# Kernel optimization log

Hardware: AMD Instinct MI355X
Metric: run time of the kernel (lower is better)

The kernel has to match this reference:

```python
import jax, jax.numpy as jnp
import numpy as np

N, E = 20000, 256000
NODE_DIM, EDGE_DIM = 128, 8
HID, HEADS, LAYERS = 64, 4, 3   # TransformerConv: out_channels per head = HID, concat=False
CLASSES, GRAPHS = 3, 64
HC = HEADS * HID


def setup_inputs() -> dict:
    key = jax.random.key(0)
    ks = iter(jax.random.split(key, 40))
    g = lambda shape, s=0.05: jax.random.normal(next(ks), shape, dtype=jnp.float32) * s
    z = lambda shape: jnp.zeros(shape, jnp.float32)
    return dict(
        x=jax.random.normal(next(ks), (N, NODE_DIM), dtype=jnp.float32),
        edge_attr=jax.random.normal(next(ks), (E, EDGE_DIM), dtype=jnp.float32),
        node_W=g((NODE_DIM, HID)), node_b=z((HID,)),
        e1_W=g((EDGE_DIM, HID)), e1_b=z((HID,)),
        e2_W=g((HID, HID)), e2_b=z((HID,)),
        Wq=g((LAYERS, HID, HC)), bq=z((LAYERS, HC)),
        Wk=g((LAYERS, HID, HC)), bk=z((LAYERS, HC)),
        Wv=g((LAYERS, HID, HC)), bv=z((LAYERS, HC)),
        We=g((LAYERS, HID, HC)),                      # lin_edge has bias=False in PyG
        Wskip=g((LAYERS, HID, HID)), bskip=z((LAYERS, HID)),
        ln_g=jnp.ones((LAYERS, HID), jnp.float32), ln_b=z((LAYERS, HID)),
        cls_W=g((HID, CLASSES)), cls_b=z((CLASSES,)),
        edge_index=jax.random.randint(next(ks), (2, E), 0, N),
        batch=jnp.sort(jax.random.randint(next(ks), (N,), 0, GRAPHS)),
    )


def _layer_norm(x, g, b, eps=1e-5):
    m = x.mean(-1, keepdims=True)
    v = x.var(-1, keepdims=True)
    return (x - m) * jax.lax.rsqrt(v + eps) * g + b


def reference(x, edge_attr, node_W, node_b, e1_W, e1_b, e2_W, e2_b,
              Wq, bq, Wk, bk, Wv, bv, We, Wskip, bskip, ln_g, ln_b,
              cls_W, cls_b, edge_index, batch):
    src, dst = edge_index[0], edge_index[1]          # messages flow src -> dst
    h = x @ node_W + node_b                          # [N, HID]
    e = jax.nn.relu(edge_attr @ e1_W + e1_b) @ e2_W + e2_b  # [E, HID]
    scale = 1.0 / jnp.sqrt(jnp.float32(HID))
    for l in range(LAYERS):                          # fixed small layer count
        res = h
        q = (h @ Wq[l] + bq[l]).reshape(N, HEADS, HID)
        k = (h @ Wk[l] + bk[l]).reshape(N, HEADS, HID)
        v = (h @ Wv[l] + bv[l]).reshape(N, HEADS, HID)
        ee = (e @ We[l]).reshape(E, HEADS, HID)      # per-layer edge projection
        kj = k[src] + ee                             # [E, H, C] irregular gather
        alpha = (q[dst] * kj).sum(-1) * scale        # [E, H]
        amax = jax.ops.segment_max(alpha, dst, num_segments=N)
        ea = jnp.exp(alpha - amax[dst])
        denom = jax.ops.segment_sum(ea, dst, num_segments=N)
        alpha = ea / denom[dst]                      # segment softmax over in-edges
        # dropout on alpha: identity in eval mode
        msg = (v[src] + ee) * alpha[..., None]       # [E, H, C]
        agg = jax.ops.segment_sum(msg, dst, num_segments=N)  # [N, H, C]
        conv = agg.mean(axis=1) + (res @ Wskip[l] + bskip[l])  # concat=False, root_weight
        h = jax.nn.relu(_layer_norm(conv + res, ln_g[l], ln_b[l]))
        # model-level dropout: identity in eval mode
    gsum = jax.ops.segment_sum(h, batch, num_segments=GRAPHS)
    gcnt = jax.ops.segment_sum(jnp.ones((N, 1), h.dtype), batch, num_segments=GRAPHS)
    pooled = gsum / jnp.maximum(gcnt, 1.0)           # global mean pool
    return jax.nn.log_softmax(pooled @ cls_W + cls_b, axis=-1)  # [GRAPHS, CLASSES]
```

## Files before the change

kernel.cpp:

```cpp
#include <hip/hip_runtime.h>
#include <hip/hip_bf16.h>
#include <math.h>

#define NN 20000
#define NE 256000
#define NODE_DIM_ 128
#define EDGE_DIM_ 8
#define HID 64
#define HEADS 4
#define NLAYERS 3
#define NCLASSES 3
#define NGRAPHS 64
#define HC 256
#define EB 64
#define EPB 16

typedef __hip_bfloat16 bf16;
using v8s = __attribute__((ext_vector_type(8))) short;
using u16x8 = __attribute__((ext_vector_type(8))) unsigned short;
using f32x4 = __attribute__((ext_vector_type(4))) float;

__device__ __forceinline__ float B2F(bf16 x) { return __bfloat162float(x); }
__device__ __forceinline__ bf16 F2B(float x) { return __float2bfloat16(x); }
__device__ __forceinline__ short F2BS(float x) {
    union { bf16 b; short s; } u; u.b = __float2bfloat16(x); return u.s;
}
__device__ __forceinline__ float U2F(unsigned short u) { return __uint_as_float(((unsigned)u) << 16); }
__device__ __forceinline__ int clampi(int x, int lo, int hi) { return min(max(x, lo), hi); }

__global__ void gt_write_const(float* out, int n, float val) {
    int i = blockIdx.x * blockDim.x + threadIdx.x;
    if (i < n) out[i] = val;
}

__global__ void gt_zero_i32(int* p, int n) {
    int i = blockIdx.x * blockDim.x + threadIdx.x;
    if (i < n) p[i] = 0;
}

__global__ void gt_prep_wqe(const float* __restrict__ Wq, const float* __restrict__ bq,
                            const float* __restrict__ bk, const float* __restrict__ bv,
                            const float* __restrict__ We,
                            float* __restrict__ Wqe, float* __restrict__ bias4) {
    int b = blockIdx.x;
    int l = b / 65, kk = b % 65;
    int t = threadIdx.x;
    int hh = t >> 6, d = t & 63;
    const float* Weh = We + (size_t)l * HID * HC + (size_t)d * HC + hh * 64;
    if (kk < 64) {
        const float* Wqr = Wq + (size_t)l * HID * HC + (size_t)kk * HC + hh * 64;
        float s = 0.f;
        for (int c = 0; c < 64; ++c) s += Wqr[c] * Weh[c];
        Wqe[(size_t)l * HID * HC + (size_t)kk * HC + t] = s;
    } else {
        const float* bqr = bq + (size_t)l * HC + hh * 64;
        float s = 0.f;
        for (int c = 0; c < 64; ++c) s += bqr[c] * Weh[c];
        bias4[(size_t)l * 1024 + 768 + t] = s;
        bias4[(size_t)l * 1024 + t]       = bq[(size_t)l * HC + t];
        bias4[(size_t)l * 1024 + 256 + t] = bk[(size_t)l * HC + t];
        bias4[(size_t)l * 1024 + 512 + t] = bv[(size_t)l * HC + t];
    }
}

__global__ void gt_pack_qkv(const float* __restrict__ Wq, const float* __restrict__ Wk,
                            const float* __restrict__ Wv, const float* __restrict__ Wqe,
                            bf16* __restrict__ Bp) {
    int idx = blockIdx.x * 256 + threadIdx.x;
    if (idx >= NLAYERS * 8192) return;
    int lane = idx & 63;
    int ks = (idx >> 6) & 1;
    int nf = (idx >> 7) & 63;
    int l = idx >> 13;
    int col = nf * 16 + (lane & 15);
    int k0 = ks * 32 + (lane >> 4) * 8;
    const float* src;
    int c;
    if (col < 256)      { src = Wq  + (size_t)l * HID * HC; c = col; }
    else if (col < 512) { src = Wk  + (size_t)l * HID * HC; c = col - 256; }
    else if (col < 768) { src = Wv  + (size_t)l * HID * HC; c = col - 512; }
    else                { src = Wqe + (size_t)l * HID * HC; c = col - 768; }
    bf16* dst = Bp + (size_t)idx * 8;
#pragma unroll
    for (int j = 0; j < 8; ++j) dst[j] = F2B(src[(size_t)(k0 + j) * HC + c]);
}

__global__ void gt_pack_w2(const float* __restrict__ W2, bf16* __restrict__ B2p) {
    int idx = blockIdx.x * 256 + threadIdx.x;
    if (idx >= 512) return;
    int lane = idx & 63;
    int ks = (idx >> 6) & 1;
    int nf = idx >> 7;
    int col = nf * 16 + (lane & 15);
    int k0 = ks * 32 + (lane >> 4) * 8;
    bf16* dst = B2p + (size_t)idx * 8;
#pragma unroll
    for (int j = 0; j < 8; ++j) dst[j] = F2B(W2[(size_t)(k0 + j) * HID + col]);
}

__global__ void gt_prep_wcomb(const float* __restrict__ We, const float* __restrict__ Wskip,
                              float* __restrict__ Wc) {
    int idx = blockIdx.x * blockDim.x + threadIdx.x;
    if (idx >= NLAYERS * 320 * 64) return;
    int l = idx / (320 * 64);
    int r = idx % (320 * 64);
    int kk = r / 64;
    int c = r % 64;
    float val;
    if (kk < 256) {
        int hh = kk >> 6, j = kk & 63;
        val = We[(size_t)l * HID * HC + (size_t)j * HC + hh * 64 + c];
    } else {
        int j = kk - 256;
        val = Wskip[(size_t)l * HID * HID + (size_t)j * HID + c];
    }
    Wc[(size_t)l * 320 * 64 + (size_t)((kk >> 2) * 64 + c) * 4 + (kk & 3)] = val;
}

__global__ void gt_node_proj(const float* __restrict__ x, const float* __restrict__ W,
                             const float* __restrict__ b, float* __restrict__ h) {
    int t = threadIdx.x;
    int n = blockIdx.x * 4 + (t >> 6);
    int c = t & 63;
    __shared__ float xr[4][NODE_DIM_];
    for (int i = t; i < 4 * NODE_DIM_; i += 256) {
        int nn = blockIdx.x * 4 + i / NODE_DIM_;
        xr[i / NODE_DIM_][i % NODE_DIM_] = (nn < NN) ? x[(size_t)nn * NODE_DIM_ + i % NODE_DIM_] : 0.f;
    }
    __syncthreads();
    if (n >= NN) return;
    float acc = 0.f;
#pragma unroll 8
    for (int j = 0; j < NODE_DIM_; ++j) acc += xr[t >> 6][j] * W[j * HID + c];
    h[(size_t)n * HID + c] = acc + b[c];
}

__global__ void gt_edge_mlp(const float* __restrict__ ea, const float* __restrict__ W1,
                            const float* __restrict__ b1, const bf16* __restrict__ B2p,
                            const float* __restrict__ b2, bf16* __restrict__ ef) {
    int t = threadIdx.x;
    int c = t & 63, slot = t >> 6;
    int e0 = blockIdx.x * EB;
    __shared__ float aS[EB][EDGE_DIM_];
    __shared__ bf16 t1s[EB * 64];
    for (int i = t; i < EB * EDGE_DIM_; i += 256) {
        ((float*)aS)[i] = ea[(size_t)e0 * EDGE_DIM_ + i];
    }
    float w1r[EDGE_DIM_];
#pragma unroll
    for (int j = 0; j < EDGE_DIM_; ++j) w1r[j] = W1[j * HID + c];
    float b1c = b1[c];
    __syncthreads();
    int cu = c >> 3, ci = c & 7;
#pragma unroll
    for (int es16 = 0; es16 < 16; ++es16) {
        int es = slot * 16 + es16;
        float acc = b1c;
#pragma unroll
        for (int j = 0; j < EDGE_DIM_; ++j) acc += aS[es][j] * w1r[j];
        int cs = ((cu ^ (es & 7)) << 3) | ci;
        t1s[es * 64 + cs] = F2B(fmaxf(acc, 0.f));
    }
    __syncthreads();
    int lane = t & 63, wave = slot;
    v8s bfr0 = *(const v8s*)(B2p + ((size_t)(wave * 2 + 0) * 64 + lane) * 8);
    v8s bfr1 = *(const v8s*)(B2p + ((size_t)(wave * 2 + 1) * 64 + lane) * 8);
    int rowA = lane & 15, kg = lane >> 4;
    f32x4 acc[4];
#pragma unroll
    for (int mf = 0; mf < 4; ++mf) acc[mf] = (f32x4){0.f, 0.f, 0.f, 0.f};
#pragma unroll
    for (int mf = 0; mf < 4; ++mf) {
        int r = mf * 16 + rowA;
        int u0 = 0 * 4 + kg, u1 = 1 * 4 + kg;
        v8s a0 = *(const v8s*)&t1s[r * 64 + ((u0 ^ (r & 7)) << 3)];
        v8s a1 = *(const v8s*)&t1s[r * 64 + ((u1 ^ (r & 7)) << 3)];
        acc[mf] = __builtin_amdgcn_mfma_f32_16x16x32_bf16(a0, bfr0, acc[mf], 0, 0, 0);
        acc[mf] = __builtin_amdgcn_mfma_f32_16x16x32_bf16(a1, bfr1, acc[mf], 0, 0, 0);
    }
    int col = wave * 16 + (lane & 15);
    float bb = b2[col];
    int rbase = (lane >> 4) * 4;
#pragma unroll
    for (int mf = 0; mf < 4; ++mf) {
#pragma unroll
        for (int reg = 0; reg < 4; ++reg) {
            int e = e0 + mf * 16 + rbase + reg;
            ef[(size_t)e * HID + col] = F2B(acc[mf][reg] + bb);
        }
    }
}

__global__ void gt_count_dst(const int* __restrict__ ei, int* cnt) {
    int e = blockIdx.x * blockDim.x + threadIdx.x;
    if (e < NE) {
        int d = clampi(ei[NE + e], 0, NN - 1);
        atomicAdd(&cnt[d], 1);
    }
}

__global__ void gt_scan_csr(const int* __restrict__ cnt, int* __restrict__ rp, int* __restrict__ cur) {
    __shared__ int part[256];
    int tid = threadIdx.x;
    const int CH = (NN + 255) / 256;
    int s0 = tid * CH, s1 = min(s0 + CH, NN);
    int s = 0;
    for (int i = s0; i < s1; ++i) s += cnt[i];
    part[tid] = s;
    __syncthreads();
    for (int off = 1; off < 256; off <<= 1) {
        int vv = (tid >= off) ? part[tid - off] : 0;
        __syncthreads();
        if (tid >= off) part[tid] += vv;
        __syncthreads();
    }
    int base = (tid == 0) ? 0 : part[tid - 1];
    for (int i = s0; i < s1; ++i) {
        rp[i] = base;
        cur[i] = base;
        base += cnt[i];
    }
    if (tid == 255) rp[NN] = part[255];
}

__global__ void gt_fill_csr(const int* __restrict__ ei, int* cur, int* csr) {
    int e = blockIdx.x * blockDim.x + threadIdx.x;
    if (e < NE) {
        int d = clampi(ei[NE + e], 0, NN - 1);
        int pos = atomicAdd(&cur[d], 1);
        if (pos >= 0 && pos < NE) csr[pos] = e;
    }
}

__global__ void __launch_bounds__(256)
gt_qkv_mfma(const float* __restrict__ h, const bf16* __restrict__ Bp,
            const float* __restrict__ bias4,
            float* __restrict__ q, bf16* __restrict__ kv, float* __restrict__ qe) {
    int t = threadIdx.x, lane = t & 63, wave = t >> 6;
    int n0 = blockIdx.x * 16;
    int rowA = lane & 15, kg = lane >> 4;

    v8s a[2];
    {
        const float* hr = h + (size_t)(n0 + rowA) * HID;
#pragma unroll
        for (int ks = 0; ks < 2; ++ks) {
            const float* p = hr + ks * 32 + kg * 8;
            float4 x0 = *(const float4*)p;
            float4 x1 = *(const float4*)(p + 4);
            v8s av;
            av[0] = F2BS(x0.x); av[1] = F2BS(x0.y); av[2] = F2BS(x0.z); av[3] = F2BS(x0.w);
            av[4] = F2BS(x1.x); av[5] = F2BS(x1.y); av[6] = F2BS(x1.z); av[7] = F2BS(x1.w);
            a[ks] = av;
        }
    }

    f32x4 acc[16];
#pragma unroll
    for (int nf = 0; nf < 16; ++nf) acc[nf] = (f32x4){0.f, 0.f, 0.f, 0.f};

#pragma unroll
    for (int nf = 0; nf < 16; ++nf) {
        int nfg = wave * 16 + nf;
        v8s b0 = *(const v8s*)(Bp + ((size_t)(nfg * 2 + 0) * 64 + lane) * 8);
        v8s b1 = *(const v8s*)(Bp + ((size_t)(nfg * 2 + 1) * 64 + lane) * 8);
        acc[nf] = __builtin_amdgcn_mfma_f32_16x16x32_bf16(a[0], b0, acc[nf], 0, 0, 0);
        acc[nf] = __builtin_amdgcn_mfma_f32_16x16x32_bf16(a[1], b1, acc[nf], 0, 0, 0);
    }

    int rbase = (lane >> 4) * 4;
#pragma unroll
    for (int nf = 0; nf < 16; ++nf) {
        int cc = nf * 16 + (lane & 15);
        float bias = bias4[wave * 256 + cc];
#pragma unroll
        for (int reg = 0; reg < 4; ++reg) {
            int n = n0 + rbase + reg;
            float val = acc[nf][reg] + bias;
            if (wave == 0)      q [(size_t)n * HC + cc] = val;
            else if (wave == 1) kv[(size_t)n * 512 + ((cc >> 2) << 3) + (cc & 3)] = F2B(val);
            else if (wave == 2) kv[(size_t)n * 512 + ((cc >> 2) << 3) + 4 + (cc & 3)] = F2B(val);
            else                qe[(size_t)n * HC + cc] = val;
        }
    }
}

__global__ void gt_attn_core(float* __restrict__ q, float* __restrict__ qe,
                             const bf16* __restrict__ kv, const bf16* __restrict__ ef,
                             const int* __restrict__ rp, const int* __restrict__ csr,
                             const int* __restrict__ ei) {
    int t = threadIdx.x;
    int lane = t & 63, wave = t >> 6;
    int n = blockIdx.x * 4 + wave;
    if (n >= NN) return;

    const float4* q4 = (const float4*)q;
    const float4* qe4 = (const float4*)qe;
    const u16x8* kv8 = (const u16x8*)kv;
    const ushort4* e4p = (const ushort4*)ef;
    int elane = lane & 15;

    float4 qv = q4[(size_t)n * 64 + lane];
    float4 qev = qe4[(size_t)n * 64 + lane];

    int s0 = clampi(rp[n], 0, NE), s1 = clampi(rp[n + 1], s0, NE);
    float m = -1e30f, lr = 0.f;
    float4 accv = make_float4(0.f, 0.f, 0.f, 0.f);
    float4 accs = make_float4(0.f, 0.f, 0.f, 0.f);

    auto process = [&](u16x8 k0, ushort4 f0, u16x8 k1, ushort4 f1, bool ok0, bool ok1) {
        float p0 = qv.x * U2F(k0[0]) + qv.y * U2F(k0[1]) + qv.z * U2F(k0[2]) + qv.w * U2F(k0[3])
                 + qev.x * U2F(f0.x) + qev.y * U2F(f0.y) + qev.z * U2F(f0.z) + qev.w * U2F(f0.w);
        float p1 = qv.x * U2F(k1[0]) + qv.y * U2F(k1[1]) + qv.z * U2F(k1[2]) + qv.w * U2F(k1[3])
                 + qev.x * U2F(f1.x) + qev.y * U2F(f1.y) + qev.z * U2F(f1.z) + qev.w * U2F(f1.w);
        p0 += __shfl_xor(p0, 8, 16);  p1 += __shfl_xor(p1, 8, 16);
        p0 += __shfl_xor(p0, 4, 16);  p1 += __shfl_xor(p1, 4, 16);
        p0 += __shfl_xor(p0, 2, 16);  p1 += __shfl_xor(p1, 2, 16);
        p0 += __shfl_xor(p0, 1, 16);  p1 += __shfl_xor(p1, 1, 16);
        p0 = ok0 ? p0 * 0.125f : -1e30f;
        p1 = ok1 ? p1 * 0.125f : -1e30f;
        float pm = fmaxf(p0, p1);
        if (__any(pm - m > 8.f)) {
            float nm = fmaxf(m, pm);
            float sc = __expf(m - nm);
            m = nm;
            lr *= sc;
            accv.x *= sc; accv.y *= sc; accv.z *= sc; accv.w *= sc;
            accs.x *= sc; accs.y *= sc; accs.z *= sc; accs.w *= sc;
        }
        float w0 = __expf(p0 - m);
        float w1 = __expf(p1 - m);
        lr += w0 + w1;
        accv.x += w0 * U2F(k0[4]) + w1 * U2F(k1[4]);
        accv.y += w0 * U2F(k0[5]) + w1 * U2F(k1[5]);
        accv.z += w0 * U2F(k0[6]) + w1 * U2F(k1[6]);
        accv.w += w0 * U2F(k0[7]) + w1 * U2F(k1[7]);
        accs.x += w0 * U2F(f0.x) + w1 * U2F(f1.x);
        accs.y += w0 * U2F(f0.y) + w1 * U2F(f1.y);
        accs.z += w0 * U2F(f0.z) + w1 * U2F(f1.z);
        accs.w += w0 * U2F(f0.w) + w1 * U2F(f1.w);
    };

    for (int base = s0; base < s1; base += 64) {
        int cnt = min(64, s1 - base);
        int eL = 0, srcL = 0;
        if (lane < cnt) {
            eL = clampi(csr[base + lane], 0, NE - 1);
            srcL = clampi(ei[eL], 0, NN - 1);
        }
        int jb = min(1, cnt - 1);
        int eA0 = __builtin_amdgcn_readlane(eL, 0), rA0 = __builtin_amdgcn_readlane(srcL, 0);
        int eA1 = __builtin_amdgcn_readlane(eL, jb), rA1 = __builtin_amdgcn_readlane(srcL, jb);
        u16x8 kvA0 = kv8[(size_t)rA0 * 64 + lane];
        u16x8 kvA1 = kv8[(size_t)rA1 * 64 + lane];
        ushort4 efA0 = e4p[(size_t)eA0 * 16 + elane];
        ushort4 efA1 = e4p[(size_t)eA1 * 16 + elane];
        u16x8 kvB0, kvB1;
        ushort4 efB0, efB1;
        for (int i = 0; i < cnt; i += 4) {
            {
                int j2 = min(i + 2, cnt - 1), j3 = min(i + 3, cnt - 1);
                int e2 = __builtin_amdgcn_readlane(eL, j2), r2 = __builtin_amdgcn_readlane(srcL, j2);
                int e3 = __builtin_amdgcn_readlane(eL, j3), r3 = __builtin_amdgcn_readlane(srcL, j3);
                kvB0 = kv8[(size_t)r2 * 64 + lane];
                kvB1 = kv8[(size_t)r3 * 64 + lane];
                efB0 = e4p[(size_t)e2 * 16 + elane];
                efB1 = e4p[(size_t)e3 * 16 + elane];
            }
            process(kvA0, efA0, kvA1, efA1, true, i + 1 < cnt);
            if (i + 4 < cnt) {
                int j4 = i + 4, j5 = min(i + 5, cnt - 1);
                int e4 = __builtin_amdgcn_readlane(eL, j4), r4 = __builtin_amdgcn_readlane(srcL, j4);
                int e5 = __builtin_amdgcn_readlane(eL, j5), r5 = __builtin_amdgcn_readlane(srcL, j5);
                kvA0 = kv8[(size_t)r4 * 64 + lane];
                kvA1 = kv8[(size_t)r5 * 64 + lane];
                efA0 = e4p[(size_t)e4 * 16 + elane];
                efA1 = e4p[(size_t)e5 * 16 + elane];
            }
            if (i + 2 < cnt) {
                process(kvB0, efB0, kvB1, efB1, true, i + 3 < cnt);
            }
        }
    }
    float inv = (s1 > s0) ? 0.25f / lr : 0.f;
    float4 rs = make_float4(accs.x * inv, accs.y * inv, accs.z * inv, accs.w * inv);
    ((float4*)q)[(size_t)n * 64 + lane] = rs;
    float4 rv = make_float4(accv.x * inv, accv.y * inv, accv.z * inv, accv.w * inv);
    rv.x += __shfl_xor(rv.x, 16, 64); rv.x += __shfl_xor(rv.x, 32, 64);
    rv.y += __shfl_xor(rv.y, 16, 64); rv.y += __shfl_xor(rv.y, 32, 64);
    rv.z += __shfl_xor(rv.z, 16, 64); rv.z += __shfl_xor(rv.z, 32, 64);
    rv.w += __shfl_xor(rv.w, 16, 64); rv.w += __shfl_xor(rv.w, 32, 64);
    if (lane < 16) ((float4*)qe)[(size_t)n * 64 + lane] = rv;
}

__global__ void gt_epilogue(const float* __restrict__ acc_s, const float* __restrict__ acc_vm,
                            const float* __restrict__ Wc, const float* __restrict__ bskip,
                            const float* __restrict__ lng, const float* __restrict__ lnb,
                            float* __restrict__ h) {
    int t = threadIdx.x;
    int c = t & 63, qw = t >> 6;
    int n0 = blockIdx.x * EPB;
    __shared__ float sK[EPB][320];
    __shared__ float sVM[EPB][64];
    const float4* as4 = (const float4*)acc_s;
    for (int i = t; i < EPB * 64; i += 256) {
        int nd = i >> 6, j4 = i & 63;
        *(float4*)&sK[nd][4 * j4] = as4[(size_t)(n0 + nd) * 64 + j4];
    }
    const float4* h4g = (const float4*)h;
    const float4* vm4 = (const float4*)acc_vm;
    for (int i = t; i < EPB * 16; i += 256) {
        int nd = i >> 4, j4 = i & 15;
        *(float4*)&sK[nd][256 + 4 * j4] = h4g[(size_t)(n0 + nd) * 16 + j4];
        *(float4*)&sVM[nd][4 * j4] = vm4[(size_t)(n0 + nd) * 64 + j4];
    }
    __syncthreads();
    int nb = qw * 4;
    const float4* r0 = (const float4*)&sK[nb][0];
    const float4* r1 = (const float4*)&sK[nb + 1][0];
    const float4* r2 = (const float4*)&sK[nb + 2][0];
    const float4* r3 = (const float4*)&sK[nb + 3][0];
    const float4* W4 = (const float4*)Wc;
    float a0 = 0.f, a1 = 0.f, a2 = 0.f, a3 = 0.f;
#pragma unroll 4
    for (int k4 = 0; k4 < 80; ++k4) {
        float4 w = W4[k4 * 64 + c];
        float4 x0 = r0[k4]; a0 += x0.x * w.x + x0.y * w.y + x0.z * w.z + x0.w * w.w;
        float4 x1 = r1[k4]; a1 += x1.x * w.x + x1.y * w.y + x1.z * w.z + x1.w * w.w;
        float4 x2 = r2[k4]; a2 += x2.x * w.x + x2.y * w.y + x2.z * w.z + x2.w * w.w;
        float4 x3 = r3[k4]; a3 += x3.x * w.x + x3.y * w.y + x3.z * w.z + x3.w * w.w;
    }
    float bsk = bskip[c], g = lng[c], bb = lnb[c];
    float y0 = a0 + sVM[nb][c] + sK[nb][256 + c] + bsk;
    float y1 = a1 + sVM[nb + 1][c] + sK[nb + 1][256 + c] + bsk;
    float y2 = a2 + sVM[nb + 2][c] + sK[nb + 2][256 + c] + bsk;
    float y3 = a3 + sVM[nb + 3][c] + sK[nb + 3][256 + c] + bsk;
    float m0 = y0, m1 = y1, m2 = y2, m3 = y3;
#pragma unroll
    for (int s = 32; s > 0; s >>= 1) {
        m0 += __shfl_xor(m0, s, 64);
        m1 += __shfl_xor(m1, s, 64);
        m2 += __shfl_xor(m2, s, 64);
        m3 += __shfl_xor(m3, s, 64);
    }
    m0 *= (1.f / HID); m1 *= (1.f / HID); m2 *= (1.f / HID); m3 *= (1.f / HID);
    float d0 = y0 - m0, d1 = y1 - m1, d2 = y2 - m2, d3 = y3 - m3;
    float v0 = d0 * d0, v1 = d1 * d1, v2 = d2 * d2, v3 = d3 * d3;
#pragma unroll
    for (int s = 32; s > 0; s >>= 1) {
        v0 += __shfl_xor(v0, s, 64);
        v1 += __shfl_xor(v1, s, 64);
        v2 += __shfl_xor(v2, s, 64);
        v3 += __shfl_xor(v3, s, 64);
    }
    v0 *= (1.f / HID); v1 *= (1.f / HID); v2 *= (1.f / HID); v3 *= (1.f / HID);
    h[(size_t)(n0 + nb) * HID + c]     = fmaxf(d0 * rsqrtf(v0 + 1e-5f) * g + bb, 0.f);
    h[(size_t)(n0 + nb + 1) * HID + c] = fmaxf(d1 * rsqrtf(v1 + 1e-5f) * g + bb, 0.f);
    h[(size_t)(n0 + nb + 2) * HID + c] = fmaxf(d2 * rsqrtf(v2 + 1e-5f) * g + bb, 0.f);
    h[(size_t)(n0 + nb + 3) * HID + c] = fmaxf(d3 * rsqrtf(v3 + 1e-5f) * g + bb, 0.f);
}

__global__ void gt_pool_sum(const float* __restrict__ h, const int* __restrict__ batch,
                            float* __restrict__ psum) {
    int t = threadIdx.x;
    int c = t & 63, slot = t >> 6;
    int n0 = blockIdx.x * 256;
    float acc = 0.f;
    int curg = -1;
    for (int i = slot; i < 256; i += 4) {
        int n = n0 + i;
        if (n >= NN) break;
        int g = clampi(batch[n], 0, NGRAPHS - 1);
        float val = h[(size_t)n * HID + c];
        if (g != curg) {
            if (curg >= 0) atomicAdd(&psum[curg * HID + c], acc);
            curg = g;
            acc = 0.f;
        }
        acc += val;
    }
    if (curg >= 0) atomicAdd(&psum[curg * HID + c], acc);
}

__global__ void gt_classify(const float* __restrict__ psum, const int* __restrict__ batch,
                            const float* __restrict__ W, const float* __restrict__ b,
                            float* __restrict__ out) {
    int g = blockIdx.x;
    int c = threadIdx.x;
    __shared__ float pooled[HID];
    __shared__ float lg[4];
    __shared__ int bounds[2];
    if (c < 2) {
        int target = g + c;
        int lo = 0, hi = NN;
        while (lo < hi) {
            int mid = (lo + hi) >> 1;
            if (batch[mid] < target) lo = mid + 1; else hi = mid;
        }
        bounds[c] = lo;
    }
    __syncthreads();
    float divf = fmaxf((float)(bounds[1] - bounds[0]), 1.f);
    pooled[c] = psum[g * HID + c] / divf;
    __syncthreads();
    if (c < NCLASSES) {
        float acc = 0.f;
        for (int j = 0; j < HID; ++j) acc += pooled[j] * W[j * NCLASSES + c];
        lg[c] = acc + b[c];
    }
    __syncthreads();
    if (c == 0) {
        float m = fmaxf(lg[0], fmaxf(lg[1], lg[2]));
        float ssum = 0.f;
        for (int cc = 0; cc < NCLASSES; ++cc) ssum += __expf(lg[cc] - m);
        float lse = logf(ssum);
        for (int cc = 0; cc < NCLASSES; ++cc) out[g * NCLASSES + cc] = lg[cc] - m - lse;
    }
}

extern "C" void kernel_launch(void* const* d_in, const int* in_sizes, int n_in,
                              void* d_out, int out_size, void* d_ws, size_t ws_size,
                              hipStream_t stream) {
    float* out = (float*)d_out;

    static const int EXPECT[23] = {2560000, 2048000, 8192, 64, 512, 64, 4096, 64,
                                   49152, 768, 49152, 768, 49152, 768, 49152,
                                   12288, 192, 192, 192, 192, 3, 512000, 20000};
    int bad = -1;
    if (n_in != 23) bad = 99;
    else {
        for (int i = 0; i < 23; ++i) {
            if (in_sizes[i] != EXPECT[i]) { bad = i; break; }
        }
    }
    if (bad >= 0) {
        float val = (bad == 99) ? 4000.f : (5000.f + 10.f * bad);
        gt_write_const<<<1, 256, 0, stream>>>(out, out_size, val);
        return;
    }

    const float* x        = (const float*)d_in[0];
    const float* edge_attr= (const float*)d_in[1];
    const float* node_W   = (const float*)d_in[2];
    const float* node_b   = (const float*)d_in[3];
    const float* e1_W     = (const float*)d_in[4];
    const float* e1_b     = (const float*)d_in[5];
    const float* e2_W     = (const float*)d_in[6];
    const float* e2_b     = (const float*)d_in[7];
    const float* Wq       = (const float*)d_in[8];
    const float* bq       = (const float*)d_in[9];
    const float* Wk       = (const float*)d_in[10];
    const float* bk       = (const float*)d_in[11];
    const float* Wv       = (const float*)d_in[12];
    const float* bv       = (const float*)d_in[13];
    const float* We       = (const float*)d_in[14];
    const float* Wskip    = (const float*)d_in[15];
    const float* bskip    = (const float*)d_in[16];
    const float* lng      = (const float*)d_in[17];
    const float* lnb      = (const float*)d_in[18];
    const float* cls_W    = (const float*)d_in[19];
    const float* cls_b    = (const float*)d_in[20];
    const int*   ei       = (const int*)d_in[21];
    const int*   batch    = (const int*)d_in[22];

    char* w = (char*)d_ws;
    auto alloc = [&](size_t bytes) -> char* {
        char* p = w;
        w += (bytes + 255) & ~(size_t)255;
        return p;
    };
    float* h     = (float*)alloc((size_t)NN * HID * 4);
    bf16*  ef    = (bf16*)alloc((size_t)NE * HID * 2);
    float* q     = (float*)alloc((size_t)NN * HC * 4);
    bf16*  kv    = (bf16*)alloc((size_t)NN * 512 * 2);
    float* qe    = (float*)alloc((size_t)NN * HC * 4);
    float* Wqe   = (float*)alloc((size_t)NLAYERS * HID * HC * 4);
    float* bias4 = (float*)alloc((size_t)NLAYERS * 1024 * 4);
    bf16*  Bp    = (bf16*)alloc((size_t)NLAYERS * 8192 * 8 * 2);
    bf16*  B2p   = (bf16*)alloc((size_t)512 * 8 * 2);
    float* Wc    = (float*)alloc((size_t)NLAYERS * 320 * 64 * 4);
    float* psum  = (float*)alloc((size_t)NGRAPHS * HID * 4);
    int*   cnt   = (int*)alloc((size_t)NN * 4);
    int*   rp    = (int*)alloc((size_t)(NN + 1) * 4);
    int*   cur   = (int*)alloc((size_t)NN * 4);
    int*   csr   = (int*)alloc((size_t)NE * 4);

    gt_node_proj<<<(NN + 3) / 4, 256, 0, stream>>>(x, node_W, node_b, h);
    gt_prep_wqe<<<NLAYERS * 65, 256, 0, stream>>>(Wq, bq, bk, bv, We, Wqe, bias4);
    gt_pack_qkv<<<(NLAYERS * 8192 + 255) / 256, 256, 0, stream>>>(Wq, Wk, Wv, Wqe, Bp);
    gt_pack_w2<<<2, 256, 0, stream>>>(e2_W, B2p);
    gt_edge_mlp<<<NE / EB, 256, 0, stream>>>(edge_attr, e1_W, e1_b, B2p, e2_b, ef);
    gt_prep_wcomb<<<(NLAYERS * 320 * 64 + 255) / 256, 256, 0, stream>>>(We, Wskip, Wc);
    gt_zero_i32<<<(NN + 255) / 256, 256, 0, stream>>>(cnt, NN);
    gt_count_dst<<<(NE + 255) / 256, 256, 0, stream>>>(ei, cnt);
    gt_scan_csr<<<1, 256, 0, stream>>>(cnt, rp, cur);
    gt_fill_csr<<<(NE + 255) / 256, 256, 0, stream>>>(ei, cur, csr);

    for (int l = 0; l < NLAYERS; ++l) {
        const bf16* Bp_l  = Bp + (size_t)l * 8192 * 8;
        const float* b4_l = bias4 + (size_t)l * 1024;
        const float* Wc_l = Wc + (size_t)l * 320 * 64;
        const float* bs_l = bskip + (size_t)l * HID;
        const float* lg_l = lng + (size_t)l * HID;
        const float* lb_l = lnb + (size_t)l * HID;

        gt_qkv_mfma<<<NN / 16, 256, 0, stream>>>(h, Bp_l, b4_l, q, kv, qe);
        gt_attn_core<<<(NN + 3) / 4, 256, 0, stream>>>(q, qe, kv, ef, rp, csr, ei);
        gt_epilogue<<<NN / EPB, 256, 0, stream>>>(q, qe, Wc_l, bs_l, lg_l, lb_l, h);
    }

    gt_zero_i32<<<(NGRAPHS * HID + 255) / 256, 256, 0, stream>>>((int*)psum, NGRAPHS * HID);
    gt_pool_sum<<<(NN + 255) / 256, 256, 0, stream>>>(h, batch, psum);
    gt_classify<<<NGRAPHS, HID, 0, stream>>>(psum, batch, cls_W, cls_b, out);
}
```

Measured before the change: 558.2 us.

## Fuse attention aggregation with skip-projection, layer norm and ReLU epilogue

Merges the attention core and the epilogue kernel into one kernel, so each wave finishes its node's aggregation in registers and LDS and then runs the combined skip/edge projection, layer norm and ReLU itself. This removes one launch per layer and the global round-trip of the aggregated buffers. The edge loop now prefetches eight edges at a time and keeps two independent accumulator sets to expose more memory-level parallelism. In exchange, register pressure rises, and the Wc weights are now read once per node rather than once per 16 nodes, though they are likely cache-resident.

```diff
diff --git a/kernel.cpp b/kernel.cpp
--- a/kernel.cpp
+++ b/kernel.cpp
@@ -13,7 +13,6 @@
 #define NGRAPHS 64
 #define HC 256
 #define EB 64
-#define EPB 16
 
 typedef __hip_bfloat16 bf16;
 using v8s = __attribute__((ext_vector_type(8))) short;
@@ -285,14 +284,18 @@
     }
 }
 
-__global__ void gt_attn_core(float* __restrict__ q, float* __restrict__ qe,
-                             const bf16* __restrict__ kv, const bf16* __restrict__ ef,
-                             const int* __restrict__ rp, const int* __restrict__ csr,
-                             const int* __restrict__ ei) {
+__global__ void gt_attn_fused(const float* __restrict__ q, const float* __restrict__ qe,
+                              const bf16* __restrict__ kv, const bf16* __restrict__ ef,
+                              const int* __restrict__ rp, const int* __restrict__ csr,
+                              const int* __restrict__ ei, const float* __restrict__ Wc,
+                              const float* __restrict__ bskip, const float* __restrict__ lng,
+                              const float* __restrict__ lnb, float* __restrict__ h) {
     int t = threadIdx.x;
     int lane = t & 63, wave = t >> 6;
     int n = blockIdx.x * 4 + wave;
-    if (n >= NN) return;
+
+    __shared__ float sS[4][320];
+    __shared__ float sVM[4][64];
 
     const float4* q4 = (const float4*)q;
     const float4* qe4 = (const float4*)qe;
@@ -302,17 +305,20 @@
 
     float4 qv = q4[(size_t)n * 64 + lane];
     float4 qev = qe4[(size_t)n * 64 + lane];
+    float resc = h[(size_t)n * HID + lane];
 
     int s0 = clampi(rp[n], 0, NE), s1 = clampi(rp[n + 1], s0, NE);
-    float m = -1e30f, lr = 0.f;
-    float4 accv = make_float4(0.f, 0.f, 0.f, 0.f);
-    float4 accs = make_float4(0.f, 0.f, 0.f, 0.f);
-
-    auto process = [&](u16x8 k0, ushort4 f0, u16x8 k1, ushort4 f1, bool ok0, bool ok1) {
-        float p0 = qv.x * U2F(k0[0]) + qv.y * U2F(k0[1]) + qv.z * U2F(k0[2]) + qv.w * U2F(k0[3])
-                 + qev.x * U2F(f0.x) + qev.y * U2F(f0.y) + qev.z * U2F(f0.z) + qev.w * U2F(f0.w);
-        float p1 = qv.x * U2F(k1[0]) + qv.y * U2F(k1[1]) + qv.z * U2F(k1[2]) + qv.w * U2F(k1[3])
-                 + qev.x * U2F(f1.x) + qev.y * U2F(f1.y) + qev.z * U2F(f1.z) + qev.w * U2F(f1.w);
+    float m = -1e30f;
+    float lrA = 0.f, lrB = 0.f;
+    float4 avA = make_float4(0.f, 0.f, 0.f, 0.f), asA = make_float4(0.f, 0.f, 0.f, 0.f);
+    float4 avB = make_float4(0.f, 0.f, 0.f, 0.f), asB = make_float4(0.f, 0.f, 0.f, 0.f);
+
+    auto proc2 = [&](const u16x8& K0, const ushort4& F0, const u16x8& K1, const ushort4& F1,
+                     bool ok0, bool ok1, float& lr_, float4& av_, float4& as_) {
+        float p0 = qv.x * U2F(K0[0]) + qv.y * U2F(K0[1]) + qv.z * U2F(K0[2]) + qv.w * U2F(K0[3])
+                 + qev.x * U2F(F0.x) + qev.y * U2F(F0.y) + qev.z * U2F(F0.z) + qev.w * U2F(F0.w);
+        float p1 = qv.x * U2F(K1[0]) + qv.y * U2F(K1[1]) + qv.z * U2F(K1[2]) + qv.w * U2F(K1[3])
+                 + qev.x * U2F(F1.x) + qev.y * U2F(F1.y) + qev.z * U2F(F1.z) + qev.w * U2F(F1.w);
         p0 += __shfl_xor(p0, 8, 16);  p1 += __shfl_xor(p1, 8, 16);
         p0 += __shfl_xor(p0, 4, 16);  p1 += __shfl_xor(p1, 4, 16);
         p0 += __shfl_xor(p0, 2, 16);  p1 += __shfl_xor(p1, 2, 16);
@@ -324,21 +330,23 @@
             float nm = fmaxf(m, pm);
             float sc = __expf(m - nm);
             m = nm;
-            lr *= sc;
-            accv.x *= sc; accv.y *= sc; accv.z *= sc; accv.w *= sc;
-            accs.x *= sc; accs.y *= sc; accs.z *= sc; accs.w *= sc;
+            lrA *= sc; lrB *= sc;
+            avA.x *= sc; avA.y *= sc; avA.z *= sc; avA.w *= sc;
+            asA.x *= sc; asA.y *= sc; asA.z *= sc; asA.w *= sc;
+            avB.x *= sc; avB.y *= sc; avB.z *= sc; avB.w *= sc;
+            asB.x *= sc; asB.y *= sc; asB.z *= sc; asB.w *= sc;
         }
         float w0 = __expf(p0 - m);
         float w1 = __expf(p1 - m);
-        lr += w0 + w1;
-        accv.x += w0 * U2F(k0[4]) + w1 * U2F(k1[4]);
-        accv.y += w0 * U2F(k0[5]) + w1 * U2F(k1[5]);
-        accv.z += w0 * U2F(k0[6]) + w1 * U2F(k1[6]);
-        accv.w += w0 * U2F(k0[7]) + w1 * U2F(k1[7]);
-        accs.x += w0 * U2F(f0.x) + w1 * U2F(f1.x);
-        accs.y += w0 * U2F(f0.y) + w1 * U2F(f1.y);
-        accs.z += w0 * U2F(f0.z) + w1 * U2F(f1.z);
-        accs.w += w0 * U2F(f0.w) + w1 * U2F(f1.w);
+        lr_ += w0 + w1;
+        av_.x += w0 * U2F(K0[4]) + w1 * U2F(K1[4]);
+        av_.y += w0 * U2F(K0[5]) + w1 * U2F(K1[5]);
+        av_.z += w0 * U2F(K0[6]) + w1 * U2F(K1[6]);
+        av_.w += w0 * U2F(K0[7]) + w1 * U2F(K1[7]);
+        as_.x += w0 * U2F(F0.x) + w1 * U2F(F1.x);
+        as_.y += w0 * U2F(F0.y) + w1 * U2F(F1.y);
+        as_.z += w0 * U2F(F0.z) + w1 * U2F(F1.z);
+        as_.w += w0 * U2F(F0.w) + w1 * U2F(F1.w);
     };
 
     for (int base = s0; base < s1; base += 64) {
@@ -348,116 +356,78 @@
             eL = clampi(csr[base + lane], 0, NE - 1);
             srcL = clampi(ei[eL], 0, NN - 1);
         }
-        int jb = min(1, cnt - 1);
-        int eA0 = __builtin_amdgcn_readlane(eL, 0), rA0 = __builtin_amdgcn_readlane(srcL, 0);
-        int eA1 = __builtin_amdgcn_readlane(eL, jb), rA1 = __builtin_amdgcn_readlane(srcL, jb);
-        u16x8 kvA0 = kv8[(size_t)rA0 * 64 + lane];
-        u16x8 kvA1 = kv8[(size_t)rA1 * 64 + lane];
-        ushort4 efA0 = e4p[(size_t)eA0 * 16 + elane];
-        ushort4 efA1 = e4p[(size_t)eA1 * 16 + elane];
-        u16x8 kvB0, kvB1;
-        ushort4 efB0, efB1;
-        for (int i = 0; i < cnt; i += 4) {
-            {
-                int j2 = min(i + 2, cnt - 1), j3 = min(i + 3, cnt - 1);
-                int e2 = __builtin_amdgcn_readlane(eL, j2), r2 = __builtin_amdgcn_readlane(srcL, j2);
-                int e3 = __builtin_amdgcn_readlane(eL, j3), r3 = __builtin_amdgcn_readlane(srcL, j3);
-                kvB0 = kv8[(size_t)r2 * 64 + lane];
-                kvB1 = kv8[(size_t)r3 * 64 + lane];
-                efB0 = e4p[(size_t)e2 * 16 + elane];
-                efB1 = e4p[(size_t)e3 * 16 + elane];
+        int i1 = min(1, cnt - 1), i2 = min(2, cnt - 1), i3 = min(3, cnt - 1);
+        int e0 = __builtin_amdgcn_readlane(eL, 0),  r0 = __builtin_amdgcn_readlane(srcL, 0);
+        int e1 = __builtin_amdgcn_readlane(eL, i1), r1 = __builtin_amdgcn_readlane(srcL, i1);
+        int e2 = __builtin_amdgcn_readlane(eL, i2), r2 = __builtin_amdgcn_readlane(srcL, i2);
+        int e3 = __builtin_amdgcn_readlane(eL, i3), r3 = __builtin_amdgcn_readlane(srcL, i3);
+        u16x8 K10 = kv8[(size_t)r0 * 64 + lane], K11 = kv8[(size_t)r1 * 64 + lane];
+        u16x8 K12 = kv8[(size_t)r2 * 64 + lane], K13 = kv8[(size_t)r3 * 64 + lane];
+        ushort4 F10 = e4p[(size_t)e0 * 16 + elane], F11 = e4p[(size_t)e1 * 16 + elane];
+        ushort4 F12 = e4p[(size_t)e2 * 16 + elane], F13 = e4p[(size_t)e3 * 16 + elane];
+        for (int i = 0; i < cnt; i += 8) {
+            int j4 = min(i + 4, cnt - 1), j5 = min(i + 5, cnt - 1);
+            int j6 = min(i + 6, cnt - 1), j7 = min(i + 7, cnt - 1);
+            int e4 = __builtin_amdgcn_readlane(eL, j4), r4 = __builtin_amdgcn_readlane(srcL, j4);
+            int e5 = __builtin_amdgcn_readlane(eL, j5), r5 = __builtin_amdgcn_readlane(srcL, j5);
+            int e6 = __builtin_amdgcn_readlane(eL, j6), r6 = __builtin_amdgcn_readlane(srcL, j6);
+            int e7 = __builtin_amdgcn_readlane(eL, j7), r7 = __builtin_amdgcn_readlane(srcL, j7);
+            u16x8 K20 = kv8[(size_t)r4 * 64 + lane], K21 = kv8[(size_t)r5 * 64 + lane];
+            u16x8 K22 = kv8[(size_t)r6 * 64 + lane], K23 = kv8[(size_t)r7 * 64 + lane];
+            ushort4 F20 = e4p[(size_t)e4 * 16 + elane], F21 = e4p[(size_t)e5 * 16 + elane];
+            ushort4 F22 = e4p[(size_t)e6 * 16 + elane], F23 = e4p[(size_t)e7 * 16 + elane];
+            proc2(K10, F10, K11, F11, true, i + 1 < cnt, lrA, avA, asA);
+            proc2(K12, F12, K13, F13, i + 2 < cnt, i + 3 < cnt, lrB, avB, asB);
+            if (i + 8 < cnt) {
+                int j9 = min(i + 9, cnt - 1), j10 = min(i + 10, cnt - 1), j11 = min(i + 11, cnt - 1);
+                int e8 = __builtin_amdgcn_readlane(eL, i + 8), r8 = __builtin_amdgcn_readlane(srcL, i + 8);
+                int e9 = __builtin_amdgcn_readlane(eL, j9),    r9 = __builtin_amdgcn_readlane(srcL, j9);
+                int eA = __builtin_amdgcn_readlane(eL, j10),   rA = __builtin_amdgcn_readlane(srcL, j10);
+                int eB = __builtin_amdgcn_readlane(eL, j11),   rB = __builtin_amdgcn_readlane(srcL, j11);
+                K10 = kv8[(size_t)r8 * 64 + lane]; K11 = kv8[(size_t)r9 * 64 + lane];
+                K12 = kv8[(size_t)rA * 64 + lane]; K13 = kv8[(size_t)rB * 64 + lane];
+                F10 = e4p[(size_t)e8 * 16 + elane]; F11 = e4p[(size_t)e9 * 16 + elane];
+                F12 = e4p[(size_t)eA * 16 + elane]; F13 = e4p[(size_t)eB * 16 + elane];
             }
-            process(kvA0, efA0, kvA1, efA1, true, i + 1 < cnt);
             if (i + 4 < cnt) {
-                int j4 = i + 4, j5 = min(i + 5, cnt - 1);
-                int e4 = __builtin_amdgcn_readlane(eL, j4), r4 = __builtin_amdgcn_readlane(srcL, j4);
-                int e5 = __builtin_amdgcn_readlane(eL, j5), r5 = __builtin_amdgcn_readlane(srcL, j5);
-                kvA0 = kv8[(size_t)r4 * 64 + lane];
-                kvA1 = kv8[(size_t)r5 * 64 + lane];
-                efA0 = e4p[(size_t)e4 * 16 + elane];
-                efA1 = e4p[(size_t)e5 * 16 + elane];
+                proc2(K20, F20, K21, F21, true, i + 5 < cnt, lrA, avA, asA);
+                proc2(K22, F22, K23, F23, i + 6 < cnt, i + 7 < cnt, lrB, avB, asB);
             }
-            if (i + 2 < cnt) {
-                process(kvB0, efB0, kvB1, efB1, true, i + 3 < cnt);
-            }
-        }
-    }
+        }
+    }
+    float lr = lrA + lrB;
     float inv = (s1 > s0) ? 0.25f / lr : 0.f;
-    float4 rs = make_float4(accs.x * inv, accs.y * inv, accs.z * inv, accs.w * inv);
-    ((float4*)q)[(size_t)n * 64 + lane] = rs;
-    float4 rv = make_float4(accv.x * inv, accv.y * inv, accv.z * inv, accv.w * inv);
+    float4 rs = make_float4((asA.x + asB.x) * inv, (asA.y + asB.y) * inv,
+                            (asA.z + asB.z) * inv, (asA.w + asB.w) * inv);
+    *(float4*)&sS[wave][4 * lane] = rs;
+    sS[wave][256 + lane] = resc;
+    float4 rv = make_float4((avA.x + avB.x) * inv, (avA.y + avB.y) * inv,
+                            (avA.z + avB.z) * inv, (avA.w + avB.w) * inv);
     rv.x += __shfl_xor(rv.x, 16, 64); rv.x += __shfl_xor(rv.x, 32, 64);
     rv.y += __shfl_xor(rv.y, 16, 64); rv.y += __shfl_xor(rv.y, 32, 64);
     rv.z += __shfl_xor(rv.z, 16, 64); rv.z += __shfl_xor(rv.z, 32, 64);
     rv.w += __shfl_xor(rv.w, 16, 64); rv.w += __shfl_xor(rv.w, 32, 64);
-    if (lane < 16) ((float4*)qe)[(size_t)n * 64 + lane] = rv;
-}
-
-__global__ void gt_epilogue(const float* __restrict__ acc_s, const float* __restrict__ acc_vm,
-                            const float* __restrict__ Wc, const float* __restrict__ bskip,
-                            const float* __restrict__ lng, const float* __restrict__ lnb,
-                            float* __restrict__ h) {
-    int t = threadIdx.x;
-    int c = t & 63, qw = t >> 6;
-    int n0 = blockIdx.x * EPB;
-    __shared__ float sK[EPB][320];
-    __shared__ float sVM[EPB][64];
-    const float4* as4 = (const float4*)acc_s;
-    for (int i = t; i < EPB * 64; i += 256) {
-        int nd = i >> 6, j4 = i & 63;
-        *(float4*)&sK[nd][4 * j4] = as4[(size_t)(n0 + nd) * 64 + j4];
-    }
-    const float4* h4g = (const float4*)h;
-    const float4* vm4 = (const float4*)acc_vm;
-    for (int i = t; i < EPB * 16; i += 256) {
-        int nd = i >> 4, j4 = i & 15;
-        *(float4*)&sK[nd][256 + 4 * j4] = h4g[(size_t)(n0 + nd) * 16 + j4];
-        *(float4*)&sVM[nd][4 * j4] = vm4[(size_t)(n0 + nd) * 64 + j4];
-    }
-    __syncthreads();
-    int nb = qw * 4;
-    const float4* r0 = (const float4*)&sK[nb][0];
-    const float4* r1 = (const float4*)&sK[nb + 1][0];
-    const float4* r2 = (const float4*)&sK[nb + 2][0];
-    const float4* r3 = (const float4*)&sK[nb + 3][0];
+    if (lane < 16) *(float4*)&sVM[wave][4 * lane] = rv;
+    __syncthreads();
     const float4* W4 = (const float4*)Wc;
-    float a0 = 0.f, a1 = 0.f, a2 = 0.f, a3 = 0.f;
+    float a = 0.f;
 #pragma unroll 4
     for (int k4 = 0; k4 < 80; ++k4) {
-        float4 w = W4[k4 * 64 + c];
-        float4 x0 = r0[k4]; a0 += x0.x * w.x + x0.y * w.y + x0.z * w.z + x0.w * w.w;
-        float4 x1 = r1[k4]; a1 += x1.x * w.x + x1.y * w.y + x1.z * w.z + x1.w * w.w;
-        float4 x2 = r2[k4]; a2 += x2.x * w.x + x2.y * w.y + x2.z * w.z + x2.w * w.w;
-        float4 x3 = r3[k4]; a3 += x3.x * w.x + x3.y * w.y + x3.z * w.z + x3.w * w.w;
-    }
-    float bsk = bskip[c], g = lng[c], bb = lnb[c];
-    float y0 = a0 + sVM[nb][c] + sK[nb][256 + c] + bsk;
-    float y1 = a1 + sVM[nb + 1][c] + sK[nb + 1][256 + c] + bsk;
-    float y2 = a2 + sVM[nb + 2][c] + sK[nb + 2][256 + c] + bsk;
-    float y3 = a3 + sVM[nb + 3][c] + sK[nb + 3][256 + c] + bsk;
-    float m0 = y0, m1 = y1, m2 = y2, m3 = y3;
-#pragma unroll
-    for (int s = 32; s > 0; s >>= 1) {
-        m0 += __shfl_xor(m0, s, 64);
-        m1 += __shfl_xor(m1, s, 64);
-        m2 += __shfl_xor(m2, s, 64);
-        m3 += __shfl_xor(m3, s, 64);
-    }
-    m0 *= (1.f / HID); m1 *= (1.f / HID); m2 *= (1.f / HID); m3 *= (1.f / HID);
-    float d0 = y0 - m0, d1 = y1 - m1, d2 = y2 - m2, d3 = y3 - m3;
-    float v0 = d0 * d0, v1 = d1 * d1, v2 = d2 * d2, v3 = d3 * d3;
-#pragma unroll
-    for (int s = 32; s > 0; s >>= 1) {
-        v0 += __shfl_xor(v0, s, 64);
-        v1 += __shfl_xor(v1, s, 64);
-        v2 += __shfl_xor(v2, s, 64);
-        v3 += __shfl_xor(v3, s, 64);
-    }
-    v0 *= (1.f / HID); v1 *= (1.f / HID); v2 *= (1.f / HID); v3 *= (1.f / HID);
-    h[(size_t)(n0 + nb) * HID + c]     = fmaxf(d0 * rsqrtf(v0 + 1e-5f) * g + bb, 0.f);
-    h[(size_t)(n0 + nb + 1) * HID + c] = fmaxf(d1 * rsqrtf(v1 + 1e-5f) * g + bb, 0.f);
-    h[(size_t)(n0 + nb + 2) * HID + c] = fmaxf(d2 * rsqrtf(v2 + 1e-5f) * g + bb, 0.f);
-    h[(size_t)(n0 + nb + 3) * HID + c] = fmaxf(d3 * rsqrtf(v3 + 1e-5f) * g + bb, 0.f);
+        float4 xk = *(const float4*)&sS[wave][4 * k4];
+        float4 w = W4[(size_t)k4 * 64 + lane];
+        a += xk.x * w.x + xk.y * w.y + xk.z * w.z + xk.w * w.w;
+    }
+    float y = a + sVM[wave][lane] + resc + bskip[lane];
+    float mm = y;
+#pragma unroll
+    for (int s = 32; s > 0; s >>= 1) mm += __shfl_xor(mm, s, 64);
+    mm *= (1.f / HID);
+    float d = y - mm;
+    float vv = d * d;
+#pragma unroll
+    for (int s = 32; s > 0; s >>= 1) vv += __shfl_xor(vv, s, 64);
+    vv *= (1.f / HID);
+    h[(size_t)n * HID + lane] = fmaxf(d * rsqrtf(vv + 1e-5f) * lng[lane] + lnb[lane], 0.f);
 }
 
 __global__ void gt_pool_sum(const float* __restrict__ h, const int* __restrict__ batch,
@@ -605,8 +575,8 @@
         const float* lb_l = lnb + (size_t)l * HID;
 
         gt_qkv_mfma<<<NN / 16, 256, 0, stream>>>(h, Bp_l, b4_l, q, kv, qe);
-        gt_attn_core<<<(NN + 3) / 4, 256, 0, stream>>>(q, qe, kv, ef, rp, csr, ei);
-        gt_epilogue<<<NN / EPB, 256, 0, stream>>>(q, qe, Wc_l, bs_l, lg_l, lb_l, h);
+        gt_attn_fused<<<NN / 4, 256, 0, stream>>>(q, qe, kv, ef, rp, csr, ei,
+                                                  Wc_l, bs_l, lg_l, lb_l, h);
     }
 
     gt_zero_i32<<<(NGRAPHS * HID + 255) / 256, 256, 0, stream>>>((int*)psum, NGRAPHS * HID);
```

After: 588.5 us. 5.4% more time.
